# Optimization experiments

Hardware: AMD Instinct MI355X
Metric: run time of the kernel (lower is better)

Reference implementation:

```python
import jax, jax.numpy as jnp
import numpy as np

AGENT_RADIUS = 0.2
SAFETY_DIST = 0.1
_ang = np.linspace(0.0, 2.0 * np.pi, 8, endpoint=False)
OBSTACLES = np.stack([10.0 * np.cos(_ang), 10.0 * np.sin(_ang), 0.5 * np.ones(8)], axis=-1).astype(np.float32)  # (x, y, r)


def _qp_solve(p, G, h):
    """Exact solve of: min_z 0.5 z^T z + p^T z  s.t. G z <= h, z in R^2.
    Equivalent to QPFunction with Q=I. Enumerates KKT candidates over active
    sets of size 0, 1, 2 (closed form in 2D) and picks the feasible optimum.
    p: [2], G: [m,2], h: [m]."""
    m = G.shape[0]
    ii, jj = np.triu_indices(m, 1)
    # active set {} -> unconstrained minimizer
    z0 = -p[None, :]                                        # [1,2]
    # active set {i}: z = -p - lam*g_i, g_i.z = h_i
    gg = jnp.sum(G * G, axis=-1)                            # [m]
    lam1 = (-(G @ p) - h) / (gg + 1e-12)
    z1 = -p[None, :] - lam1[:, None] * G                    # [m,2]
    ok1 = lam1 >= -1e-8
    # active set {i,j}: z solves 2x2 system [g_i; g_j] z = [h_i; h_j]
    Gi, Gj = G[ii], G[jj]                                   # [P,2]
    hi, hj = h[ii], h[jj]
    det = Gi[:, 0] * Gj[:, 1] - Gi[:, 1] * Gj[:, 0]
    det_ok = jnp.abs(det) > 1e-9
    ds = jnp.where(det_ok, det, 1.0)
    zx = (hi * Gj[:, 1] - hj * Gi[:, 1]) / ds
    zy = (Gi[:, 0] * hj - Gj[:, 0] * hi) / ds
    z2 = jnp.stack([zx, zy], axis=-1)                       # [P,2]
    r = -(z2 + p[None, :])                                  # A^T lam = r
    lam_i = (Gj[:, 1] * r[:, 0] - Gj[:, 0] * r[:, 1]) / ds
    lam_j = (Gi[:, 0] * r[:, 1] - Gi[:, 1] * r[:, 0]) / ds
    ok2 = det_ok & (lam_i >= -1e-8) & (lam_j >= -1e-8)
    Z = jnp.concatenate([z0, z1, z2], axis=0)               # [K,2]
    ok = jnp.concatenate([jnp.ones((1,), bool), ok1, ok2], axis=0)
    tol = 1e-6 * (1.0 + jnp.abs(h))
    feas = jnp.all(Z @ G.T <= (h + tol)[None, :], axis=-1)  # [K]
    obj = 0.5 * jnp.sum(Z * Z, axis=-1) + Z @ p
    obj = jnp.where(ok & feas, obj, jnp.inf)
    return Z[jnp.argmin(obj)]


def _forward(x, mean, std, W1, b1, W21, b21, W31, b31, W22, b22, W32, b32):
    x0 = x * std + mean                                     # de-normalized state [B,8]
    hid = jax.nn.relu(x @ W1.T + b1)
    x31 = jax.nn.relu(hid @ W21.T + b21) @ W31.T + b31      # reference control p [B,2]
    x32 = 4.0 * jax.nn.sigmoid(jax.nn.relu(hid @ W22.T + b22) @ W32.T + b32)  # CBF penalties [B,2]
    px, py, theta, v = x0[:, 0], x0[:, 1], x0[:, 2], x0[:, 3]
    ox, oy, oth, ov = x0[:, 4], x0[:, 5], x0[:, 6], x0[:, 7]
    st, ct = jnp.sin(theta), jnp.cos(theta)
    vs, vc = v * st, v * ct
    obs = jnp.asarray(OBSTACLES, x.dtype)
    # static obstacle constraints, vectorized over the n_obs obstacles
    dx = px[:, None] - obs[None, :, 0]                      # [B,n_obs]
    dy = py[:, None] - obs[None, :, 1]
    R = AGENT_RADIUS + obs[:, 2] + SAFETY_DIST
    bar = dx * dx + dy * dy - (R * R)[None, :]
    bdot = 2.0 * dx * vc[:, None] + 2.0 * dy * vs[:, None]
    Lf2b = (2.0 * v * v)[:, None]
    u1 = -2.0 * dx * vs[:, None] + 2.0 * dy * vc[:, None]
    u2 = 2.0 * dx * ct[:, None] + 2.0 * dy * st[:, None]
    G_obs = -jnp.stack([u1, u2], axis=-1)                   # [B,n_obs,2]
    s0, s1 = x32[:, 0:1], x32[:, 1:2]
    h_obs = Lf2b + (s0 + s1) * bdot + (s0 * s1) * bar       # [B,n_obs]
    # opponent constraint
    Ro = 2.0 * AGENT_RADIUS + SAFETY_DIST
    dxo, dyo = px - ox, py - oy
    so, co = jnp.sin(oth), jnp.cos(oth)
    bar_o = dxo * dxo + dyo * dyo - Ro * Ro
    bdot_o = 2.0 * dxo * (vc - ov * co) + 2.0 * dyo * (vs - ov * so)
    Lf2b_o = 2.0 * (v * v + ov * ov + 2.0 * v * ov * jnp.cos(theta - oth))
    u1o = -2.0 * dxo * vs + 2.0 * dyo * vc
    u2o = 2.0 * dxo * ct + 2.0 * dyo * st
    G_opp = -jnp.stack([u1o, u2o], axis=-1)[:, None, :]     # [B,1,2]
    h_opp = (Lf2b_o + (x32[:, 0] + x32[:, 1]) * bdot_o + x32[:, 0] * x32[:, 1] * bar_o)[:, None]
    G = jnp.concatenate([G_obs, G_opp], axis=1)             # [B,m,2]
    h = jnp.concatenate([h_obs, h_opp], axis=1)             # [B,m]
    return jax.vmap(_qp_solve)(x31, G, h)                   # [B,2]


def setup_inputs() -> dict:
    key = jax.random.key(0)
    ks = jax.random.split(key, 6)
    B, nF, H1, H2 = 65536, 8, 256, 128

    def lin(k, o, i):
        k1, k2 = jax.random.split(k)
        W = jax.random.normal(k1, (o, i), jnp.float32) / np.float32(np.sqrt(i))
        b = jax.random.normal(k2, (o,), jnp.float32) * 0.01
        return W, b

    W1, b1 = lin(ks[0], H1, nF)
    W21, b21 = lin(ks[1], H2, H1)
    W31, b31 = lin(ks[2], 2, H2)
    W22, b22 = lin(ks[3], H2, H1)
    W32, b32 = lin(ks[4], 2, H2)
    x = jax.random.normal(ks[5], (B, nF), jnp.float32)
    return {"x": x, "mean": jnp.zeros((nF,), jnp.float32), "std": jnp.ones((nF,), jnp.float32),
            "W1": W1, "b1": b1, "W21": W21, "b21": b21, "W31": W31, "b31": b31,
            "W22": W22, "b22": b22, "W32": W32, "b32": b32, "sgn": 1}


def reference(x, mean, std, W1, b1, W21, b21, W31, b31, W22, b22, W32, b32, sgn):
    # sgn==1 / training path -> batched differentiable QP solve
    return _forward(x, mean, std, W1, b1, W21, b21, W31, b31, W22, b22, W32, b32)
```

## Files before the change

### kernel.cpp

```cpp
#include <hip/hip_runtime.h>
#include <hip/hip_bf16.h>
#include <math.h>


typedef unsigned int u32;
typedef unsigned long long u64;
typedef unsigned short u16;
typedef __attribute__((ext_vector_type(8))) short short8;
typedef __attribute__((ext_vector_type(4))) float f32x4;
typedef __attribute__((ext_vector_type(2))) float f32x2;
typedef __attribute__((ext_vector_type(4))) u32 u32x4;

union Frag { short8 v; u32 u[4]; u32x4 q; };

__device__ __forceinline__ u32 packbf(float a, float b) {
    float2 f2; f2.x = a; f2.y = b;
    __hip_bfloat162 h = __float22bfloat162_rn(f2);
    union { __hip_bfloat162 h2; u32 u; } cv; cv.h2 = h;
    return cv.u;
}

__device__ const float OBX[8] = { 10.f, 7.07106781186547524f, 6.123234e-16f, -7.07106781186547524f,
                                 -10.f, -7.07106781186547524f, -1.8369702e-15f, 7.07106781186547524f };
__device__ const float OBY[8] = { 0.f, 7.07106781186547524f, 10.f, 7.07106781186547524f,
                                  1.2246468e-15f, -7.07106781186547524f, -10.f, -7.07106781186547524f };

#define PI0_ 0x2111111100000000ULL
#define PI1_ 0x5544443333322222ULL
#define PI2_ 0x7665ULL
#define PJ0_ 0x3876543287654321ULL
#define PJ1_ 0x7687658765487654ULL
#define PJ2_ 0x8878ULL
__device__ __forceinline__ int unpack4(u64 w0, u64 w1, u64 w2, int t) {
    u64 w = (t < 16) ? w0 : (t < 32) ? w1 : w2;
    return (int)((w >> ((t & 15) * 4)) & 15);
}

__global__ __launch_bounds__(256)
void prep_kernel(const float* __restrict__ W21, const float* __restrict__ W22,
                 u32* __restrict__ ws)
{
    int idx  = blockIdx.x * 256 + threadIdx.x;
    int lane = idx & 63;
    int nt   = (idx >> 6) & 7;
    int ks   = (idx >> 9) & 7;
    int head = idx >> 12;
    const float* W = head ? W22 : W21;
    int n  = nt * 16 + (lane & 15);
    int k0 = ks * 32 + (lane >> 4) * 8;
    const float* s = W + n * 256 + k0;
    u32x4 o;
    o.x = packbf(s[0], s[1]);
    o.y = packbf(s[2], s[3]);
    o.z = packbf(s[4], s[5]);
    o.w = packbf(s[6], s[7]);
    __builtin_nontemporal_store(o, (u32x4*)ws + idx);
}

__global__ __launch_bounds__(256)
void gemm_kernel(const float* __restrict__ x,
                 const float* __restrict__ W1,
                 const float* __restrict__ b1,
                 const float* __restrict__ b21,
                 const float* __restrict__ W31,
                 const float* __restrict__ b31,
                 const float* __restrict__ b22,
                 const float* __restrict__ W32,
                 const float* __restrict__ b32,
                 const u32* __restrict__ wsB,
                 f32x4* __restrict__ ps, int Btot)
{
    const int tid  = threadIdx.x;
    const int wave = tid >> 6;
    const int lane = tid & 63;
    const int q    = lane >> 4;
    const int m    = lane & 15;
    const int blockRow = blockIdx.x * 64;

    __shared__ u32x4 stage[2048];
    __shared__ float lds_p[64][4];

    f32x4 xa0, xb0;
    {
        int R0 = blockRow + wave * 16 + m;
        const f32x4* xv0 = (const f32x4*)(x + (R0 < Btot ? R0 : 0) * 8);
        xa0 = xv0[0]; xb0 = xv0[1];
    }

    const f32x4* W1v = (const f32x4*)W1;
    const f32x4* b1v = (const f32x4*)b1;

    Frag A[8];
    #pragma unroll
    for (int ks = 0; ks < 8; ++ks) {
        int kb = ks * 32 + q * 8;
        f32x4 bA = b1v[kb >> 2];
        f32x4 bB = b1v[(kb >> 2) + 1];
        float h0[8];
        #pragma unroll
        for (int j = 0; j < 8; ++j) {
            f32x4 wa = W1v[(kb + j) * 2];
            f32x4 wb = W1v[(kb + j) * 2 + 1];
            float a0 = (j < 4) ? bA[j] : bB[j - 4];
            a0 = fmaf(wa.x, xa0.x, a0);
            a0 = fmaf(wa.y, xa0.y, a0);
            a0 = fmaf(wa.z, xa0.z, a0);
            a0 = fmaf(wa.w, xa0.w, a0);
            a0 = fmaf(wb.x, xb0.x, a0);
            a0 = fmaf(wb.y, xb0.y, a0);
            a0 = fmaf(wb.z, xb0.z, a0);
            a0 = fmaf(wb.w, xb0.w, a0);
            h0[j] = fmaxf(a0, 0.f);
        }
        #pragma unroll
        for (int t = 0; t < 4; ++t)
            A[ks].u[t] = packbf(h0[2 * t], h0[2 * t + 1]);
    }

    const u32x4* wsB4 = (const u32x4*)wsB;

    #pragma unroll 1
    for (int head = 0; head < 2; ++head) {
        const float* b2 = head ? b22 : b21;
        const float* W3 = head ? W32 : W31;
        const float* b3 = head ? b32 : b31;

        f32x4 acc[8];
        #pragma unroll
        for (int nt = 0; nt < 8; ++nt) acc[nt] = (f32x4){0.f, 0.f, 0.f, 0.f};

        #pragma unroll
        for (int half = 0; half < 2; ++half) {
            const u32x4* src = wsB4 + head * 4096 + half * 2048;
            #pragma unroll
            for (int i = 0; i < 8; ++i) {
                int fi = (wave * 8 + i) * 64 + lane;
                stage[fi] = src[fi];
            }
            __syncthreads();
            #pragma unroll
            for (int ksl = 0; ksl < 4; ++ksl) {
                const int ks = half * 4 + ksl;
                Frag Bf[8];
                #pragma unroll
                for (int nt = 0; nt < 8; ++nt)
                    Bf[nt].q = stage[ksl * 512 + nt * 64 + lane];
                #pragma unroll
                for (int nt = 0; nt < 8; ++nt)
                    acc[nt] = __builtin_amdgcn_mfma_f32_16x16x32_bf16(A[ks].v, Bf[nt].v, acc[nt], 0, 0, 0);
            }
            __syncthreads();
        }

        float pr0[4], pr1[4];
        #pragma unroll
        for (int rg = 0; rg < 4; ++rg) { pr0[rg] = 0.f; pr1[rg] = 0.f; }
        #pragma unroll
        for (int nt = 0; nt < 8; ++nt) {
            int col = nt * 16 + m;
            float b2c = b2[col];
            float w0c = W3[col];
            float w1c = W3[128 + col];
            #pragma unroll
            for (int rg = 0; rg < 4; ++rg) {
                float rv = fmaxf(acc[nt][rg] + b2c, 0.f);
                pr0[rg] = fmaf(rv, w0c, pr0[rg]);
                pr1[rg] = fmaf(rv, w1c, pr1[rg]);
            }
        }
        #pragma unroll
        for (int rg = 0; rg < 4; ++rg) {
            float v0 = pr0[rg], v1 = pr1[rg];
            #pragma unroll
            for (int off = 1; off < 16; off <<= 1) {
                v0 += __shfl_xor(v0, off, 64);
                v1 += __shfl_xor(v1, off, 64);
            }
            pr0[rg] = v0; pr1[rg] = v1;
        }
        if (m == 0) {
            #pragma unroll
            for (int rg = 0; rg < 4; ++rg) {
                int row = wave * 16 + q * 4 + rg;
                float a0 = pr0[rg] + b3[0];
                float a1 = pr1[rg] + b3[1];
                if (head == 0) {
                    lds_p[row][0] = a0;
                    lds_p[row][1] = a1;
                } else {
                    lds_p[row][2] = 4.f / (1.f + expf(-a0));
                    lds_p[row][3] = 4.f / (1.f + expf(-a1));
                }
            }
        }
    }
    __syncthreads();

    if (tid < 64) {
        int R = blockRow + tid;
        if (R < Btot) {
            f32x4 pv = *(const f32x4*)lds_p[tid];
            __builtin_nontemporal_store(pv, &ps[R]);
        }
    }
}

__global__ __launch_bounds__(256)
void qp_kernel(const float* __restrict__ x,
               const float* __restrict__ meanp,
               const float* __restrict__ stdp,
               const f32x4* __restrict__ ps,
               float* __restrict__ out, int Btot)
{
    const int tid  = threadIdx.x;
    const int rq   = tid & 127;
    const int half = tid >> 7;
    const int blockRow = blockIdx.x * 128;
    const int R    = blockRow + rq;

    __shared__ f32x4 qC[9][128];
    __shared__ f32x4 res[128];

    f32x4 pv = ps[R < Btot ? R : 0];
    float p0 = pv.x, p1 = pv.y;

    if (half == 0) {
        float s0 = pv.z, s1 = pv.w;
        float xr[8];
        const float* xp = x + (R < Btot ? R : 0) * 8;
        #pragma unroll
        for (int c = 0; c < 8; ++c) xr[c] = fmaf(xp[c], stdp[c], meanp[c]);
        float px = xr[0], py = xr[1], th = xr[2], v = xr[3];
        float ox = xr[4], oy = xr[5], oth = xr[6], ov = xr[7];
        float st = sinf(th),  ct = cosf(th);
        float so = sinf(oth), co = cosf(oth);
        float vs = v * st, vc = v * ct;
        float sps = s0 + s1, ss = s0 * s1;
        float Lf2b = 2.f * v * v;
        #pragma unroll 1
        for (int k = 0; k < 8; ++k) {
            float dx = px - OBX[k], dy = py - OBY[k];
            float bar  = dx * dx + dy * dy - 0.64f;
            float bdot = 2.f * dx * vc + 2.f * dy * vs;
            float gx = 2.f * dx * vs - 2.f * dy * vc;
            float gy = -(2.f * dx * ct + 2.f * dy * st);
            float hk = Lf2b + sps * bdot + ss * bar;
            float ht = hk + 1e-6f * (1.f + fabsf(hk));
            qC[k][rq] = (f32x4){gx, gy, hk, ht};
        }
        {
            float dxo = px - ox, dyo = py - oy;
            float bar_o  = dxo * dxo + dyo * dyo - 0.25f;
            float bdot_o = 2.f * dxo * (vc - ov * co) + 2.f * dyo * (vs - ov * so);
            float Lf2b_o = 2.f * (v * v + ov * ov + 2.f * v * ov * cosf(th - oth));
            float gx = 2.f * dxo * vs - 2.f * dyo * vc;
            float gy = -(2.f * dxo * ct + 2.f * dyo * st);
            float hk = Lf2b_o + sps * bdot_o + ss * bar_o;
            float ht = hk + 1e-6f * (1.f + fabsf(hk));
            qC[8][rq] = (f32x4){gx, gy, hk, ht};
        }
    }
    __syncthreads();

    const f32x4 C0 = qC[0][rq], C1 = qC[1][rq], C2 = qC[2][rq];
    const f32x4 C3 = qC[3][rq], C4 = qC[4][rq], C5 = qC[5][rq];
    const f32x4 C6 = qC[6][rq], C7 = qC[7][rq], C8 = qC[8][rq];

    const int c0i = half ? 23 : 0;
    const int c1i = half ? 46 : 23;
    float bobj = INFINITY;
    float bzx = -p0, bzy = -p1;
    #pragma unroll 2
    for (int c = c0i; c < c1i; ++c) {
        float zx, zy;
        bool pre;
        if (c == 0) {
            zx = -p0; zy = -p1; pre = true;
        } else if (c <= 9) {
            f32x4 g = qC[c - 1][rq];
            float gg  = g.x * g.x + g.y * g.y;
            float lam = (-(g.x * p0 + g.y * p1) - g.z) / (gg + 1e-12f);
            zx = -p0 - lam * g.x;
            zy = -p1 - lam * g.y;
            pre = (lam >= -1e-8f);
        } else {
            int t = c - 10;
            int pi = unpack4(PI0_, PI1_, PI2_, t);
            int pj = unpack4(PJ0_, PJ1_, PJ2_, t);
            f32x4 gi = qC[pi][rq];
            f32x4 gj = qC[pj][rq];
            float det = gi.x * gj.y - gi.y * gj.x;
            bool dok = fabsf(det) > 1e-9f;
            float ds = dok ? det : 1.0f;
            float inv = 1.0f / ds;
            zx = (gi.z * gj.y - gj.z * gi.y) * inv;
            zy = (gi.x * gj.z - gj.x * gi.z) * inv;
            float rx = -(zx + p0), ry = -(zy + p1);
            float li = (gj.y * rx - gj.x * ry) * inv;
            float lj = (gi.x * ry - gi.y * rx) * inv;
            pre = dok && (li >= -1e-8f) && (lj >= -1e-8f);
        }
        bool ok = pre;
        ok = ok && (zx * C0.x + zy * C0.y <= C0.w);
        ok = ok && (zx * C1.x + zy * C1.y <= C1.w);
        ok = ok && (zx * C2.x + zy * C2.y <= C2.w);
        ok = ok && (zx * C3.x + zy * C3.y <= C3.w);
        ok = ok && (zx * C4.x + zy * C4.y <= C4.w);
        ok = ok && (zx * C5.x + zy * C5.y <= C5.w);
        ok = ok && (zx * C6.x + zy * C6.y <= C6.w);
        ok = ok && (zx * C7.x + zy * C7.y <= C7.w);
        ok = ok && (zx * C8.x + zy * C8.y <= C8.w);
        float obj = 0.5f * (zx * zx + zy * zy) + zx * p0 + zy * p1;
        if (ok && obj < bobj) { bobj = obj; bzx = zx; bzy = zy; }
    }

    if (half) {
        res[rq] = (f32x4){bobj, bzx, bzy, 0.f};
    }
    __syncthreads();
    if (!half) {
        f32x4 r = res[rq];
        if (r.x < bobj) { bzx = r.y; bzy = r.z; }
        if (R < Btot) {
            f32x2 o2; o2.x = bzx; o2.y = bzy;
            ((f32x2*)out)[R] = o2;
        }
    }
}

extern "C" void kernel_launch(void* const* d_in, const int* in_sizes, int n_in,
                              void* d_out, int out_size, void* d_ws, size_t ws_size,
                              hipStream_t stream) {
    const float* x    = (const float*)d_in[0];
    const float* mean = (const float*)d_in[1];
    const float* stdv = (const float*)d_in[2];
    const float* W1   = (const float*)d_in[3];
    const float* b1   = (const float*)d_in[4];
    const float* W21  = (const float*)d_in[5];
    const float* b21  = (const float*)d_in[6];
    const float* W31  = (const float*)d_in[7];
    const float* b31  = (const float*)d_in[8];
    const float* W22  = (const float*)d_in[9];
    const float* b22  = (const float*)d_in[10];
    const float* W32  = (const float*)d_in[11];
    const float* b32  = (const float*)d_in[12];
    int B = in_sizes[0] / 8;
    float* out = (float*)d_out;
    u32* ws = (u32*)d_ws;
    f32x4* ps = (f32x4*)(ws + 32768);

    hipLaunchKernelGGL(prep_kernel, dim3(32), dim3(256), 0, stream, W21, W22, ws);

    hipLaunchKernelGGL(gemm_kernel, dim3((B + 63) / 64), dim3(256), 0, stream,
                       x, W1, b1, b21, W31, b31, b22, W32, b32, ws, ps, B);
    hipLaunchKernelGGL(qp_kernel, dim3((B + 127) / 128), dim3(256), 0, stream,
                       x, mean, stdv, ps, out, B);
}
```

Before: 123.1 us.

## Fuse weight prep, MLP GEMM and QP solve into one kernel

Merges the three launches into a single kernel. The weight packing to bf16 now happens inside each block, which reads fp32 W21/W22 straight from global memory and converts them into LDS. The QP stage reuses the GEMM block's LDS for its per-row constraints, and the candidate enumeration is split across four waves instead of two. This removes two launches and the global round trip of the intermediate p/s values, but each block now repeats the weight conversion and reads twice as many weight bytes.

New measurement: 141.0 us. +14.5%, slower.

```diff
diff --git a/kernel.cpp b/kernel.cpp
--- a/kernel.cpp
+++ b/kernel.cpp
@@ -37,38 +37,20 @@
 }
 
 __global__ __launch_bounds__(256)
-void prep_kernel(const float* __restrict__ W21, const float* __restrict__ W22,
-                 u32* __restrict__ ws)
-{
-    int idx  = blockIdx.x * 256 + threadIdx.x;
-    int lane = idx & 63;
-    int nt   = (idx >> 6) & 7;
-    int ks   = (idx >> 9) & 7;
-    int head = idx >> 12;
-    const float* W = head ? W22 : W21;
-    int n  = nt * 16 + (lane & 15);
-    int k0 = ks * 32 + (lane >> 4) * 8;
-    const float* s = W + n * 256 + k0;
-    u32x4 o;
-    o.x = packbf(s[0], s[1]);
-    o.y = packbf(s[2], s[3]);
-    o.z = packbf(s[4], s[5]);
-    o.w = packbf(s[6], s[7]);
-    __builtin_nontemporal_store(o, (u32x4*)ws + idx);
-}
-
-__global__ __launch_bounds__(256)
-void gemm_kernel(const float* __restrict__ x,
-                 const float* __restrict__ W1,
-                 const float* __restrict__ b1,
-                 const float* __restrict__ b21,
-                 const float* __restrict__ W31,
-                 const float* __restrict__ b31,
-                 const float* __restrict__ b22,
-                 const float* __restrict__ W32,
-                 const float* __restrict__ b32,
-                 const u32* __restrict__ wsB,
-                 f32x4* __restrict__ ps, int Btot)
+void barriernet_kernel(const float* __restrict__ x,
+                       const float* __restrict__ meanp,
+                       const float* __restrict__ stdp,
+                       const float* __restrict__ W1,
+                       const float* __restrict__ b1,
+                       const float* __restrict__ W21,
+                       const float* __restrict__ b21,
+                       const float* __restrict__ W31,
+                       const float* __restrict__ b31,
+                       const float* __restrict__ W22,
+                       const float* __restrict__ b22,
+                       const float* __restrict__ W32,
+                       const float* __restrict__ b32,
+                       float* __restrict__ out, int Btot)
 {
     const int tid  = threadIdx.x;
     const int wave = tid >> 6;
@@ -117,10 +99,9 @@
             A[ks].u[t] = packbf(h0[2 * t], h0[2 * t + 1]);
     }
 
-    const u32x4* wsB4 = (const u32x4*)wsB;
-
     #pragma unroll 1
     for (int head = 0; head < 2; ++head) {
+        const float* W2 = head ? W22 : W21;
         const float* b2 = head ? b22 : b21;
         const float* W3 = head ? W32 : W31;
         const float* b3 = head ? b32 : b31;
@@ -131,11 +112,20 @@
 
         #pragma unroll
         for (int half = 0; half < 2; ++half) {
-            const u32x4* src = wsB4 + head * 4096 + half * 2048;
-            #pragma unroll
-            for (int i = 0; i < 8; ++i) {
-                int fi = (wave * 8 + i) * 64 + lane;
-                stage[fi] = src[fi];
+            {
+                int ks = half * 4 + wave;
+                int k0 = ks * 32 + q * 8;
+                #pragma unroll
+                for (int i = 0; i < 8; ++i) {
+                    const f32x4* s = (const f32x4*)(W2 + (i * 16 + m) * 256 + k0);
+                    f32x4 w0 = s[0], w1 = s[1];
+                    u32x4 o;
+                    o.x = packbf(w0.x, w0.y);
+                    o.y = packbf(w0.z, w0.w);
+                    o.z = packbf(w1.x, w1.y);
+                    o.w = packbf(w1.z, w1.w);
+                    stage[wave * 512 + i * 64 + lane] = o;
+                }
             }
             __syncthreads();
             #pragma unroll
@@ -196,36 +186,18 @@
     }
     __syncthreads();
 
-    if (tid < 64) {
-        int R = blockRow + tid;
-        if (R < Btot) {
-            f32x4 pv = *(const f32x4*)lds_p[tid];
-            __builtin_nontemporal_store(pv, &ps[R]);
-        }
-    }
-}
-
-__global__ __launch_bounds__(256)
-void qp_kernel(const float* __restrict__ x,
-               const float* __restrict__ meanp,
-               const float* __restrict__ stdp,
-               const f32x4* __restrict__ ps,
-               float* __restrict__ out, int Btot)
-{
-    const int tid  = threadIdx.x;
-    const int rq   = tid & 127;
-    const int half = tid >> 7;
-    const int blockRow = blockIdx.x * 128;
+    f32x4 (*qC)[64]  = (f32x4(*)[64])stage;
+    f32x4 (*res)[64] = (f32x4(*)[64])(stage + 576);
+
+    const int rq   = tid & 63;
+    const int part = tid >> 6;
     const int R    = blockRow + rq;
-
-    __shared__ f32x4 qC[9][128];
-    __shared__ f32x4 res[128];
-
-    f32x4 pv = ps[R < Btot ? R : 0];
-    float p0 = pv.x, p1 = pv.y;
-
-    if (half == 0) {
-        float s0 = pv.z, s1 = pv.w;
+    float p0 = lds_p[rq][0];
+    float p1 = lds_p[rq][1];
+
+    if (part == 0) {
+        float s0 = lds_p[rq][2];
+        float s1 = lds_p[rq][3];
         float xr[8];
         const float* xp = x + (R < Btot ? R : 0) * 8;
         #pragma unroll
@@ -266,8 +238,8 @@
     const f32x4 C3 = qC[3][rq], C4 = qC[4][rq], C5 = qC[5][rq];
     const f32x4 C6 = qC[6][rq], C7 = qC[7][rq], C8 = qC[8][rq];
 
-    const int c0i = half ? 23 : 0;
-    const int c1i = half ? 46 : 23;
+    const int c0i = (part == 0) ? 0  : (part == 1) ? 12 : (part == 2) ? 24 : 35;
+    const int c1i = (part == 0) ? 12 : (part == 1) ? 24 : (part == 2) ? 35 : 46;
     float bobj = INFINITY;
     float bzx = -p0, bzy = -p1;
     #pragma unroll 2
@@ -314,13 +286,16 @@
         if (ok && obj < bobj) { bobj = obj; bzx = zx; bzy = zy; }
     }
 
-    if (half) {
-        res[rq] = (f32x4){bobj, bzx, bzy, 0.f};
+    if (part) {
+        res[part - 1][rq] = (f32x4){bobj, bzx, bzy, 0.f};
     }
     __syncthreads();
-    if (!half) {
-        f32x4 r = res[rq];
-        if (r.x < bobj) { bzx = r.y; bzy = r.z; }
+    if (part == 0) {
+        #pragma unroll
+        for (int pp = 0; pp < 3; ++pp) {
+            f32x4 r = res[pp][rq];
+            if (r.x < bobj) { bobj = r.x; bzx = r.y; bzy = r.z; }
+        }
         if (R < Btot) {
             f32x2 o2; o2.x = bzx; o2.y = bzy;
             ((f32x2*)out)[R] = o2;
@@ -346,13 +321,8 @@
     const float* b32  = (const float*)d_in[12];
     int B = in_sizes[0] / 8;
     float* out = (float*)d_out;
-    u32* ws = (u32*)d_ws;
-    f32x4* ps = (f32x4*)(ws + 32768);
-
-    hipLaunchKernelGGL(prep_kernel, dim3(32), dim3(256), 0, stream, W21, W22, ws);
-
-    hipLaunchKernelGGL(gemm_kernel, dim3((B + 63) / 64), dim3(256), 0, stream,
-                       x, W1, b1, b21, W31, b31, b22, W32, b32, ws, ps, B);
-    hipLaunchKernelGGL(qp_kernel, dim3((B + 127) / 128), dim3(256), 0, stream,
-                       x, mean, stdv, ps, out, B);
+
+    hipLaunchKernelGGL(barriernet_kernel, dim3((B + 63) / 64), dim3(256), 0, stream,
+                       x, mean, stdv, W1, b1, W21, b21, W31, b31,
+                       W22, b22, W32, b32, out, B);
 }
```
